# Performance work log

Hardware: AMD Instinct MI355X
Metric: run time of the kernel (lower is better)

The kernel has to match this reference:

```python
import jax, jax.numpy as jnp
import numpy as np

N = 50000       # nodes
E = 800000      # edges
IN = 256        # input channels
H = 4           # heads
C = 64          # hidden channels per head
NEG_SLOPE = 0.2 # PyG GATConv default LeakyReLU slope
EPS = 1e-16


def setup_inputs() -> dict:
    key = jax.random.key(0)
    k_x, k_e, k_w, k_as, k_ad = jax.random.split(key, 5)
    x = jax.random.normal(k_x, (N, IN), dtype=jnp.float32)
    edge_index = jax.random.randint(k_e, (2, E), 0, N, dtype=jnp.int64)
    # GATConv params: glorot-style scale
    W = jax.random.normal(k_w, (IN, H * C), dtype=jnp.float32) * (1.0 / np.sqrt(IN))
    att_src = jax.random.normal(k_as, (H, C), dtype=jnp.float32) * (1.0 / np.sqrt(C))
    att_dst = jax.random.normal(k_ad, (H, C), dtype=jnp.float32) * (1.0 / np.sqrt(C))
    return {"x": x, "edge_index": edge_index, "W": W, "att_src": att_src, "att_dst": att_dst}


def reference(x, edge_index, W, att_src, att_dst):
    src, dst = edge_index[0], edge_index[1]
    # linear projection, split heads: [N, H, C]
    xh = (x @ W).reshape(N, H, C)
    # per-node attention halves: [N, H]
    a_src = jnp.einsum('nhc,hc->nh', xh, att_src)
    a_dst = jnp.einsum('nhc,hc->nh', xh, att_dst)
    # per-edge logits with LeakyReLU: [E, H]
    alpha = a_src[src] + a_dst[dst]
    alpha = jnp.where(alpha >= 0, alpha, NEG_SLOPE * alpha)
    # segment softmax over destination nodes
    m = jax.ops.segment_max(alpha, dst, num_segments=N)          # [N, H]
    ex = jnp.exp(alpha - m[dst])                                  # [E, H]
    denom = jax.ops.segment_sum(ex, dst, num_segments=N)         # [N, H]
    att = ex / (denom[dst] + EPS)                                 # [E, H]
    # weighted message scatter-add: [N, H, C] -> concat heads [N, H*C]
    msg = att[:, :, None] * xh[src]                               # [E, H, C]
    out = jax.ops.segment_sum(msg, dst, num_segments=N)
    out = out.reshape(N, H * C)
    return (out, att)
```

## Files before the change

kernel.cpp:

```cpp
#include <hip/hip_runtime.h>
#include <math.h>

#define IN_CH   256
#define HC      256
#define H_HEADS 4
#define NEG_SLOPE 0.2f
#define LOG2E   1.44269504088896f
#define MINIT   -3.0e38f

typedef __attribute__((ext_vector_type(8))) short short8;
typedef __attribute__((ext_vector_type(4))) float float4v;
typedef __attribute__((ext_vector_type(2))) float float2v;

__device__ __forceinline__ float bf2f(unsigned short b) {
    return __uint_as_float(((unsigned)b) << 16);
}
__device__ __forceinline__ unsigned short f2bf(float f) {
    unsigned u = __float_as_uint(f);
    u += 0x7fffu + ((u >> 16) & 1u);
    return (unsigned short)(u >> 16);
}
__device__ __forceinline__ float lrelu(float a) {
    return a >= 0.f ? a : NEG_SLOPE * a;
}
__device__ __forceinline__ float fexp2(float a) {
    return __builtin_amdgcn_exp2f(a);
}


__global__ void prep_w(const float* __restrict__ w,
                       unsigned short* __restrict__ wt) {
    int idx = blockIdx.x * 256 + threadIdx.x;
    int k = idx >> 8, c = idx & 255;
    wt[(size_t)c * 256 + k] = f2bf(w[idx]);
}

__global__ __launch_bounds__(256) void gemm_xh(const float* __restrict__ x,
                                               const unsigned short* __restrict__ wt,
                                               const float* __restrict__ att_s,
                                               const float* __restrict__ att_d,
                                               unsigned short* __restrict__ xh_pl,
                                               float* __restrict__ a_src,
                                               float* __restrict__ a_dst, int N) {
    __shared__ __attribute__((aligned(16))) unsigned char lds_a[16384];
    int tid  = threadIdx.x;
    int wave = tid >> 6;
    int lane = tid & 63;
    int quad = lane >> 4;
    int l16  = lane & 15;
    int rb   = blockIdx.x * 16;

#pragma unroll
    for (int pass = 0; pass < 2; ++pass) {
        int s  = pass * 256 + tid;
        int kc = s >> 4;
        int m  = s & 15;
        int grow = rb + m; if (grow >= N) grow = N - 1;
        const float* gp = x + (size_t)grow * IN_CH + kc * 8;
        float4v f0 = *(const float4v*)gp;
        float4v f1 = *(const float4v*)(gp + 4);
        short8 hi, lo;
#pragma unroll
        for (int j = 0; j < 4; ++j) {
            unsigned short h0 = f2bf(f0[j]);
            hi[j] = (short)h0;
            lo[j] = (short)f2bf(f0[j] - bf2f(h0));
            unsigned short h1 = f2bf(f1[j]);
            hi[4 + j] = (short)h1;
            lo[4 + j] = (short)f2bf(f1[j] - bf2f(h1));
        }
        *(short8*)(lds_a + (size_t)s * 16) = hi;
        *(short8*)(lds_a + 8192 + (size_t)s * 16) = lo;
    }
    __syncthreads();

    float4v acc[4] = {};
    const unsigned short* wt_base = wt + ((size_t)wave * 64 + l16) * IN_CH;
#pragma unroll
    for (int k0 = 0; k0 < 8; ++k0) {
        int kc   = k0 * 4 + quad;
        int slot = kc * 16 + l16;
        short8 a_hi = *(const short8*)(lds_a + slot * 16);
        short8 a_lo = *(const short8*)(lds_a + 8192 + slot * 16);
#pragma unroll
        for (int ct = 0; ct < 4; ++ct) {
            short8 bh = *(const short8*)(wt_base + (size_t)ct * 16 * IN_CH
                                         + k0 * 32 + quad * 8);
            acc[ct] = __builtin_amdgcn_mfma_f32_16x16x32_bf16(a_lo, bh, acc[ct], 0, 0, 0);
            acc[ct] = __builtin_amdgcn_mfma_f32_16x16x32_bf16(a_hi, bh, acc[ct], 0, 0, 0);
        }
    }

    int cb = wave;
    float ps[4] = {0.f, 0.f, 0.f, 0.f};
    float pd[4] = {0.f, 0.f, 0.f, 0.f};
#pragma unroll
    for (int ct = 0; ct < 4; ++ct) {
        float as_c = att_s[cb * 64 + ct * 16 + l16] * LOG2E;
        float ad_c = att_d[cb * 64 + ct * 16 + l16] * LOG2E;
        int ch = cb * 64 + ct * 16 + l16;
        int pl = ch >> 5, wc = ch & 31;
#pragma unroll
        for (int r = 0; r < 4; ++r) {
            float v = acc[ct][r];
            int grow = rb + quad * 4 + r;
            if (grow < N)
                xh_pl[((size_t)pl * N + grow) * 32 + wc] = f2bf(v);
            ps[r] += v * as_c;
            pd[r] += v * ad_c;
        }
    }
#pragma unroll
    for (int off = 1; off < 16; off <<= 1) {
#pragma unroll
        for (int r = 0; r < 4; ++r) {
            ps[r] += __shfl_xor(ps[r], off);
            pd[r] += __shfl_xor(pd[r], off);
        }
    }
    if (l16 == 0) {
#pragma unroll
        for (int r = 0; r < 4; ++r) {
            int grow = rb + quad * 4 + r;
            if (grow < N) {
                a_src[(size_t)grow * 4 + cb] = ps[r];
                a_dst[(size_t)grow * 4 + cb] = pd[r];
            }
        }
    }
}

__global__ __launch_bounds__(256) void deg_count(const int* __restrict__ ei,
                                                 int* __restrict__ deg, int E) {
    int e = blockIdx.x * 256 + threadIdx.x;
    if (e >= E) return;
    atomicAdd(deg + ei[E + e], 1);
}

__global__ __launch_bounds__(256) void scan_part(const int* __restrict__ deg,
                                                 int* __restrict__ part, int N) {
    int t = threadIdx.x;
    int base = blockIdx.x * 1024 + t * 4;
    int s = 0;
    if (base + 4 <= N) {
        int4 v = *(const int4*)(deg + base);
        s = v.x + v.y + v.z + v.w;
    } else {
#pragma unroll
        for (int j = 0; j < 4; ++j)
            if (base + j < N) s += deg[base + j];
    }
#pragma unroll
    for (int off = 1; off < 64; off <<= 1) s += __shfl_xor(s, off);
    __shared__ int ws[4];
    if ((t & 63) == 0) ws[t >> 6] = s;
    __syncthreads();
    if (t == 0) part[blockIdx.x] = ws[0] + ws[1] + ws[2] + ws[3];
}

__global__ __launch_bounds__(256) void scan_final(const int* __restrict__ deg,
                                                  const int* __restrict__ part,
                                                  int* __restrict__ rowptr,
                                                  int* __restrict__ cursor, int N) {
    __shared__ int sm[256];
    __shared__ int wsum[4];
    int t = threadIdx.x;
    int bacc = 0;
    for (int j = t; j < blockIdx.x; j += 256) bacc += part[j];
#pragma unroll
    for (int off = 1; off < 64; off <<= 1) bacc += __shfl_xor(bacc, off);
    if ((t & 63) == 0) wsum[t >> 6] = bacc;

    int base = blockIdx.x * 1024 + t * 4;
    int v0 = 0, v1 = 0, v2 = 0, v3 = 0;
    if (base + 4 <= N) {
        int4 v = *(const int4*)(deg + base);
        v0 = v.x; v1 = v.y; v2 = v.z; v3 = v.w;
    } else {
        if (base + 0 < N) v0 = deg[base + 0];
        if (base + 1 < N) v1 = deg[base + 1];
        if (base + 2 < N) v2 = deg[base + 2];
        if (base + 3 < N) v3 = deg[base + 3];
    }
    int s = v0 + v1 + v2 + v3;
    sm[t] = s;
    __syncthreads();
    for (int off = 1; off < 256; off <<= 1) {
        int tmp = (t >= off) ? sm[t - off] : 0;
        __syncthreads();
        sm[t] += tmp;
        __syncthreads();
    }
    int boff = wsum[0] + wsum[1] + wsum[2] + wsum[3];
    int run = boff + sm[t] - s;
    int r0 = run, r1 = r0 + v0, r2 = r1 + v1, r3 = r2 + v2;
    if (base + 4 <= N) {
        *(int4*)(rowptr + base) = (int4){r0, r1, r2, r3};
        *(int4*)(cursor + base) = (int4){r0, r1, r2, r3};
    } else {
        if (base + 0 < N) { rowptr[base + 0] = r0; cursor[base + 0] = r0; }
        if (base + 1 < N) { rowptr[base + 1] = r1; cursor[base + 1] = r1; }
        if (base + 2 < N) { rowptr[base + 2] = r2; cursor[base + 2] = r2; }
        if (base + 3 < N) { rowptr[base + 3] = r3; cursor[base + 3] = r3; }
    }
}

__global__ __launch_bounds__(256) void fill_csr(const int* __restrict__ ei,
                                                int* __restrict__ cursor,
                                                int* __restrict__ csr_off6, int E) {
    int e = blockIdx.x * 256 + threadIdx.x;
    if (e >= E) return;
    int s = ei[e], d = ei[E + e];
    int slot = atomicAdd(cursor + d, 1);
    csr_off6[slot] = s << 6;
}

__global__ __launch_bounds__(256) void softmax_stats(const int* __restrict__ csr_off6,
                                                     const float* __restrict__ a_src,
                                                     const float* __restrict__ a_dst,
                                                     const int* __restrict__ rowptr,
                                                     const int* __restrict__ deg,
                                                     float* __restrict__ pack, int N) {
    int d = blockIdx.x * 256 + threadIdx.x;
    int h = blockIdx.y;
    if (d >= N) return;
    int start = rowptr[d], cnt = deg[d];
    float adh = a_dst[(size_t)d * 4 + h];
    const int* offs = csr_off6 + start;
    float m = MINIT, l = 0.f;
    for (int i = 0; i < cnt; ++i) {
        int off = offs[i];
        float al = lrelu(a_src[(off >> 4) + h] + adh);
        float mn = fmaxf(m, al);
        l = l * fexp2(m - mn) + fexp2(al - mn);
        m = mn;
    }
    pack[(size_t)d * 8 + h]     = m;
    pack[(size_t)d * 8 + 4 + h] = 1.f / (l + 1e-16f);
}

__global__ __launch_bounds__(256) void gat_planes(const int* __restrict__ csr_off6,
                                                  const float* __restrict__ a_src,
                                                  const float* __restrict__ a_dst,
                                                  const int* __restrict__ rowptr,
                                                  const int* __restrict__ deg,
                                                  const unsigned short* __restrict__ xh_pl,
                                                  const float* __restrict__ pack,
                                                  float* __restrict__ out, int N) {
    int tid = threadIdx.x;
    int g   = blockIdx.x & 7;
    int db  = blockIdx.x >> 3;
    int grp = tid >> 4;
    int l16 = tid & 15;
    int d   = db * 16 + grp;
    bool dv = d < N;
    int dc  = dv ? d : N - 1;
    int start = rowptr[dc];
    int cnt   = dv ? deg[dc] : 0;
    int h = g >> 1;

    int cw = cnt;
    cw = max(cw, __shfl_xor(cw, 16));
    cw = max(cw, __shfl_xor(cw, 32));

    const char* pb = (const char*)xh_pl + (size_t)g * N * 64;
    int lb = l16 * 4;
    float adh = a_dst[(size_t)dc * 4 + h];
    float m   = pack[(size_t)dc * 8 + h];
    float inv = pack[(size_t)dc * 8 + 4 + h];

    float aE0 = 0.f, aE1 = 0.f, aO0 = 0.f, aO1 = 0.f;

#define POFF(i) (((i) < cnt) ? csr_off6[start + (i)] : 0)

    int oE = POFF(0), oO = POFF(1);
    int oE1 = POFF(2), oO1 = POFF(3);
    float asE = a_src[(oE >> 4) + h], asO = a_src[(oO >> 4) + h];

#pragma unroll 2
    for (int i = 0; i < cw; i += 2) {
        unsigned xE = *(const unsigned*)(pb + (size_t)(unsigned)oE + lb);
        unsigned xO = *(const unsigned*)(pb + (size_t)(unsigned)oO + lb);
        int oE2 = POFF(i + 4), oO2 = POFF(i + 5);
        float asEn = a_src[(oE1 >> 4) + h], asOn = a_src[(oO1 >> 4) + h];

        float alE = (i < cnt)     ? lrelu(asE + adh) : -INFINITY;
        float alO = (i + 1 < cnt) ? lrelu(asO + adh) : -INFINITY;
        float pE = fexp2(alE - m);
        float pO = fexp2(alO - m);
        aE0 += pE * bf2f((unsigned short)(xE & 0xffffu));
        aE1 += pE * bf2f((unsigned short)(xE >> 16));
        aO0 += pO * bf2f((unsigned short)(xO & 0xffffu));
        aO1 += pO * bf2f((unsigned short)(xO >> 16));

        oE = oE1; oO = oO1; oE1 = oE2; oO1 = oO2;
        asE = asEn; asO = asOn;
    }
#undef POFF

    if (dv) {
        float2v o;
        o[0] = (aE0 + aO0) * inv;
        o[1] = (aE1 + aO1) * inv;
        *(float2v*)(out + (size_t)d * HC + g * 32 + l16 * 2) = o;
    }
}

__global__ __launch_bounds__(256) void att_edge(const int* __restrict__ ei,
                                                const float* __restrict__ a_src,
                                                const float* __restrict__ a_dst,
                                                const float* __restrict__ pack,
                                                float* __restrict__ att_out, int E) {
    int e = blockIdx.x * 256 + threadIdx.x;
    if (e >= E) return;
    int s = ei[e], d = ei[E + e];
    float4v as = *(const float4v*)(a_src + (size_t)s * 4);
    float4v ad = *(const float4v*)(a_dst + (size_t)d * 4);
    float4v mm = *(const float4v*)(pack + (size_t)d * 8);
    float4v gg = *(const float4v*)(pack + (size_t)d * 8 + 4);
    float4v o;
#pragma unroll
    for (int h = 0; h < 4; ++h)
        o[h] = fexp2(lrelu(as[h] + ad[h]) - mm[h]) * gg[h];
    *(float4v*)(att_out + (size_t)e * 4) = o;
}

extern "C" void kernel_launch(void* const* d_in, const int* in_sizes, int n_in,
                              void* d_out, int out_size, void* d_ws, size_t ws_size,
                              hipStream_t stream) {
    const float* x     = (const float*)d_in[0];
    const int*   ei    = (const int*)d_in[1];
    const float* W     = (const float*)d_in[2];
    const float* att_s = (const float*)d_in[3];
    const float* att_d = (const float*)d_in[4];

    const int N = in_sizes[0] / IN_CH;
    const int E = in_sizes[1] / 2;

    char* ws = (char*)d_ws;
    size_t off = 0;
    unsigned short* xh_pl = (unsigned short*)(ws + off); off += (size_t)N * HC * 2;
    unsigned short* wt    = (unsigned short*)(ws + off); off += (size_t)IN_CH * HC * 2;
    float* a_src = (float*)(ws + off); off += (size_t)N * H_HEADS * 4;
    float* a_dst = (float*)(ws + off); off += (size_t)N * H_HEADS * 4;
    float* pack  = (float*)(ws + off); off += (size_t)N * 8 * 4;
    int* rowptr  = (int*)(ws + off); off += (size_t)N * 4;
    int* cursor  = (int*)(ws + off); off += (size_t)N * 4;
    int* csr_off6 = (int*)(ws + off); off += (size_t)E * 4;
    int* part    = (int*)(ws + off); off += 1024 * 4;
    size_t zoff = off;
    int* deg     = (int*)(ws + off); off += (size_t)N * 4;

    float* out     = (float*)d_out;
    float* out_att = out + (size_t)N * HC;

    (void)hipMemsetAsync(ws + zoff, 0, off - zoff, stream);

    const int NB  = (N + 1023) / 1024;
    const int NDB = (N + 15) / 16;

    prep_w<<<256, 256, 0, stream>>>(W, wt);
    deg_count<<<(E + 255) / 256, 256, 0, stream>>>(ei, deg, E);
    gemm_xh<<<(N + 15) / 16, 256, 0, stream>>>(x, wt, att_s, att_d,
                                               xh_pl, a_src, a_dst, N);
    scan_part<<<NB, 256, 0, stream>>>(deg, part, N);
    scan_final<<<NB, 256, 0, stream>>>(deg, part, rowptr, cursor, N);
    fill_csr<<<(E + 255) / 256, 256, 0, stream>>>(ei, cursor, csr_off6, E);
    softmax_stats<<<dim3((N + 255) / 256, 4), 256, 0, stream>>>(csr_off6, a_src, a_dst,
                                                                rowptr, deg, pack, N);
    gat_planes<<<NDB * 8, 256, 0, stream>>>(csr_off6, a_src, a_dst, rowptr, deg,
                                            xh_pl, pack, out, N);
    att_edge<<<(E + 255) / 256, 256, 0, stream>>>(ei, a_src, a_dst, pack,
                                                  out_att, E);
}
```

Measured before the change: 370.0 us.

## Precompute normalized edge attention in softmax pass and widen gather per lane

```diff
diff --git a/kernel.cpp b/kernel.cpp
--- a/kernel.cpp
+++ b/kernel.cpp
@@ -10,10 +10,16 @@
 
 typedef __attribute__((ext_vector_type(8))) short short8;
 typedef __attribute__((ext_vector_type(4))) float float4v;
-typedef __attribute__((ext_vector_type(2))) float float2v;
+typedef __attribute__((ext_vector_type(2))) unsigned uint2v;
 
 __device__ __forceinline__ float bf2f(unsigned short b) {
     return __uint_as_float(((unsigned)b) << 16);
+}
+__device__ __forceinline__ float blo(unsigned u) {
+    return __uint_as_float(u << 16);
+}
+__device__ __forceinline__ float bhi(unsigned u) {
+    return __uint_as_float(u & 0xffff0000u);
 }
 __device__ __forceinline__ unsigned short f2bf(float f) {
     unsigned u = __float_as_uint(f);
@@ -220,7 +226,9 @@
                                                      const float* __restrict__ a_dst,
                                                      const int* __restrict__ rowptr,
                                                      const int* __restrict__ deg,
-                                                     float* __restrict__ pack, int N) {
+                                                     float* __restrict__ pack,
+                                                     float* __restrict__ p_soa,
+                                                     int N, int E) {
     int d = blockIdx.x * 256 + threadIdx.x;
     int h = blockIdx.y;
     if (d >= N) return;
@@ -235,24 +243,29 @@
         l = l * fexp2(m - mn) + fexp2(al - mn);
         m = mn;
     }
+    float inv = 1.f / (l + 1e-16f);
     pack[(size_t)d * 8 + h]     = m;
-    pack[(size_t)d * 8 + 4 + h] = 1.f / (l + 1e-16f);
+    pack[(size_t)d * 8 + 4 + h] = inv;
+    float* pout = p_soa + (size_t)h * E + start;
+    for (int i = 0; i < cnt; ++i) {
+        int off = offs[i];
+        float al = lrelu(a_src[(off >> 4) + h] + adh);
+        pout[i] = fexp2(al - m) * inv;
+    }
 }
 
 __global__ __launch_bounds__(256) void gat_planes(const int* __restrict__ csr_off6,
-                                                  const float* __restrict__ a_src,
-                                                  const float* __restrict__ a_dst,
+                                                  const float* __restrict__ p_soa,
                                                   const int* __restrict__ rowptr,
                                                   const int* __restrict__ deg,
                                                   const unsigned short* __restrict__ xh_pl,
-                                                  const float* __restrict__ pack,
-                                                  float* __restrict__ out, int N) {
+                                                  float* __restrict__ out, int N, int E) {
     int tid = threadIdx.x;
     int g   = blockIdx.x & 7;
     int db  = blockIdx.x >> 3;
-    int grp = tid >> 4;
-    int l16 = tid & 15;
-    int d   = db * 16 + grp;
+    int grp = tid >> 3;
+    int l8  = tid & 7;
+    int d   = db * 32 + grp;
     bool dv = d < N;
     int dc  = dv ? d : N - 1;
     int start = rowptr[dc];
@@ -260,49 +273,46 @@
     int h = g >> 1;
 
     int cw = cnt;
+    cw = max(cw, __shfl_xor(cw, 8));
     cw = max(cw, __shfl_xor(cw, 16));
     cw = max(cw, __shfl_xor(cw, 32));
 
     const char* pb = (const char*)xh_pl + (size_t)g * N * 64;
-    int lb = l16 * 4;
-    float adh = a_dst[(size_t)dc * 4 + h];
-    float m   = pack[(size_t)dc * 8 + h];
-    float inv = pack[(size_t)dc * 8 + 4 + h];
-
-    float aE0 = 0.f, aE1 = 0.f, aO0 = 0.f, aO1 = 0.f;
+    const float* ph = p_soa + (size_t)h * E + start;
+    int lb = l8 * 8;
+
+    float a0 = 0.f, a1 = 0.f, a2 = 0.f, a3 = 0.f;
 
 #define POFF(i) (((i) < cnt) ? csr_off6[start + (i)] : 0)
-
-    int oE = POFF(0), oO = POFF(1);
-    int oE1 = POFF(2), oO1 = POFF(3);
-    float asE = a_src[(oE >> 4) + h], asO = a_src[(oO >> 4) + h];
+#define PPV(i)  (((i) < cnt) ? ph[i] : 0.f)
+
+    int   oE  = POFF(0), oO  = POFF(1);
+    float pE  = PPV(0),  pO  = PPV(1);
+    int   oE1 = POFF(2), oO1 = POFF(3);
+    float pE1 = PPV(2),  pO1 = PPV(3);
 
 #pragma unroll 2
     for (int i = 0; i < cw; i += 2) {
-        unsigned xE = *(const unsigned*)(pb + (size_t)(unsigned)oE + lb);
-        unsigned xO = *(const unsigned*)(pb + (size_t)(unsigned)oO + lb);
-        int oE2 = POFF(i + 4), oO2 = POFF(i + 5);
-        float asEn = a_src[(oE1 >> 4) + h], asOn = a_src[(oO1 >> 4) + h];
-
-        float alE = (i < cnt)     ? lrelu(asE + adh) : -INFINITY;
-        float alO = (i + 1 < cnt) ? lrelu(asO + adh) : -INFINITY;
-        float pE = fexp2(alE - m);
-        float pO = fexp2(alO - m);
-        aE0 += pE * bf2f((unsigned short)(xE & 0xffffu));
-        aE1 += pE * bf2f((unsigned short)(xE >> 16));
-        aO0 += pO * bf2f((unsigned short)(xO & 0xffffu));
-        aO1 += pO * bf2f((unsigned short)(xO >> 16));
+        uint2v xE = *(const uint2v*)(pb + (size_t)(unsigned)oE + lb);
+        uint2v xO = *(const uint2v*)(pb + (size_t)(unsigned)oO + lb);
+        int   oE2 = POFF(i + 4), oO2 = POFF(i + 5);
+        float pE2 = PPV(i + 4),  pO2 = PPV(i + 5);
+
+        a0 += pE * blo(xE[0]); a1 += pE * bhi(xE[0]);
+        a2 += pE * blo(xE[1]); a3 += pE * bhi(xE[1]);
+        a0 += pO * blo(xO[0]); a1 += pO * bhi(xO[0]);
+        a2 += pO * blo(xO[1]); a3 += pO * bhi(xO[1]);
 
         oE = oE1; oO = oO1; oE1 = oE2; oO1 = oO2;
-        asE = asEn; asO = asOn;
+        pE = pE1; pO = pO1; pE1 = pE2; pO1 = pO2;
     }
 #undef POFF
+#undef PPV
 
     if (dv) {
-        float2v o;
-        o[0] = (aE0 + aO0) * inv;
-        o[1] = (aE1 + aO1) * inv;
-        *(float2v*)(out + (size_t)d * HC + g * 32 + l16 * 2) = o;
+        float4v o;
+        o[0] = a0; o[1] = a1; o[2] = a2; o[3] = a3;
+        *(float4v*)(out + (size_t)d * HC + g * 32 + l8 * 4) = o;
     }
 }
 
@@ -347,6 +357,7 @@
     int* rowptr  = (int*)(ws + off); off += (size_t)N * 4;
     int* cursor  = (int*)(ws + off); off += (size_t)N * 4;
     int* csr_off6 = (int*)(ws + off); off += (size_t)E * 4;
+    float* p_soa = (float*)(ws + off); off += (size_t)E * 4 * 4;
     int* part    = (int*)(ws + off); off += 1024 * 4;
     size_t zoff = off;
     int* deg     = (int*)(ws + off); off += (size_t)N * 4;
@@ -357,7 +368,7 @@
     (void)hipMemsetAsync(ws + zoff, 0, off - zoff, stream);
 
     const int NB  = (N + 1023) / 1024;
-    const int NDB = (N + 15) / 16;
+    const int NDB = (N + 31) / 32;
 
     prep_w<<<256, 256, 0, stream>>>(W, wt);
     deg_count<<<(E + 255) / 256, 256, 0, stream>>>(ei, deg, E);
@@ -367,9 +378,10 @@
     scan_final<<<NB, 256, 0, stream>>>(deg, part, rowptr, cursor, N);
     fill_csr<<<(E + 255) / 256, 256, 0, stream>>>(ei, cursor, csr_off6, E);
     softmax_stats<<<dim3((N + 255) / 256, 4), 256, 0, stream>>>(csr_off6, a_src, a_dst,
-                                                                rowptr, deg, pack, N);
-    gat_planes<<<NDB * 8, 256, 0, stream>>>(csr_off6, a_src, a_dst, rowptr, deg,
-                                            xh_pl, pack, out, N);
+                                                                rowptr, deg, pack,
+                                                                p_soa, N, E);
+    gat_planes<<<NDB * 8, 256, 0, stream>>>(csr_off6, p_soa, rowptr, deg,
+                                            xh_pl, out, N, E);
     att_edge<<<(E + 255) / 256, 256, 0, stream>>>(ei, a_src, a_dst, pack,
                                                   out_att, E);
 }
```

Measured after the change: 391.5 us. +5.8%, slower.
